# Kernel tuning notes

Measured on AMD Instinct MI355X. Metric: run time of the kernel, lower is better.

Reference implementation:

```python
import jax, jax.numpy as jnp
import numpy as np

NUM_HEADS = 16


def setup_inputs() -> dict:
    key = jax.random.key(0)
    k1, k2, k3 = jax.random.split(key, 3)
    B, L, H = 2, 2048, 1024
    return {
        "key": jax.random.normal(k1, (B, L, H), dtype=jnp.float32),
        "W_ctx": jax.random.normal(k2, (H, H), dtype=jnp.float32) * (1.0 / np.sqrt(H)),
        "b_ctx": jax.random.normal(k3, (H,), dtype=jnp.float32) * 0.01,
    }


def reference(key, W_ctx, b_ctx):
    # Note: the torch module defines q/k/v Linear layers but never calls them
    # in forward(); it reshapes the raw input into heads directly.
    B, L, H = key.shape
    dh = H // NUM_HEADS
    # [B, L, H] -> [B, nh, L, dh]
    x = key.reshape(B, L, NUM_HEADS, dh).transpose(0, 2, 1, 3)
    # QK^T then scale by sqrt(head_dim) (key.shape[-1] after head split)
    scores = jnp.einsum("bhqd,bhkd->bhqk", x, x) * (1.0 / np.float32(np.sqrt(dh)))
    attn = jax.nn.softmax(scores, axis=-1)  # dropout p treated as eval/identity
    ctx = jnp.einsum("bhqk,bhkd->bhqd", attn, x)
    # [B, nh, L, dh] -> [B, L, H]
    ctx = ctx.transpose(0, 2, 1, 3).reshape(B, L, H)
    # context_transform: nn.Linear(H, H, bias=True)
    return ctx @ W_ctx.T + b_ctx
```

## Files before the change

kernel.cpp:

```cpp
#include <hip/hip_runtime.h>
#include <stdint.h>

#define NH     16
#define LSEQ   2048
#define DH     64
#define HDIM   1024
#define BATCH  2

typedef __attribute__((ext_vector_type(8))) short bf16x8;
typedef __attribute__((ext_vector_type(4))) short bf16x4;
typedef __attribute__((ext_vector_type(8))) unsigned short u16x8;
typedef __attribute__((ext_vector_type(4))) float f32x4;

static __device__ inline unsigned short f2bs(float f) {
    union { float f; uint32_t u; } v; v.f = f;
    uint32_t u = v.u;
    return (unsigned short)((u + 0x7FFFu + ((u >> 16) & 1u)) >> 16);
}

#define GLOAD_LDS(gp, lp) \
    __builtin_amdgcn_global_load_lds((const __attribute__((address_space(1))) void*)(gp), \
                                     (__attribute__((address_space(3))) void*)(lp), 16, 0, 0)

#define QK_SCALE 0.42466083f

__global__ __launch_bounds__(256) void prep_kernel(const float* __restrict__ x,
                                                   const float* __restrict__ W,
                                                   unsigned short* __restrict__ xb,
                                                   unsigned short* __restrict__ xt,
                                                   unsigned short* __restrict__ wbt) {
    const int lt = blockIdx.x, bh = blockIdx.y;
    const int bid = bh * 32 + lt;
    const int t = threadIdx.x;

    if (t < 128) {
        const int gid = bid * 128 + t;
        const int n  = gid >> 7;
        const int kc = gid & 127;
        const float* src = W + (size_t)n * 1024 + kc * 8;
        float4 f0 = *(const float4*)(src);
        float4 f1 = *(const float4*)(src + 4);
        u16x8 v;
        v[0]=f2bs(f0.x); v[1]=f2bs(f0.y); v[2]=f2bs(f0.z); v[3]=f2bs(f0.w);
        v[4]=f2bs(f1.x); v[5]=f2bs(f1.y); v[6]=f2bs(f1.z); v[7]=f2bs(f1.w);
        const int nt = n >> 7, rn = n & 127;
        const int kt = kc >> 3, c = kc & 7;
        *(u16x8*)(wbt + (((size_t)nt * 16 + kt) * 128 + rn) * 64 + ((c ^ (rn & 7)) * 8)) = v;
    }

    const int b = bh >> 4, h = bh & 15;
    const int r = t >> 2, cp = t & 3;

    __shared__ __align__(16) unsigned short Sm[64][72];

    const float* src = x + ((size_t)(b * LSEQ + lt * 64 + r)) * HDIM + h * DH + cp * 16;
    float4 f0 = *(const float4*)(src);
    float4 f1 = *(const float4*)(src + 4);
    float4 f2 = *(const float4*)(src + 8);
    float4 f3 = *(const float4*)(src + 12);
    u16x8 lo, hi;
    lo[0]=f2bs(f0.x); lo[1]=f2bs(f0.y); lo[2]=f2bs(f0.z); lo[3]=f2bs(f0.w);
    lo[4]=f2bs(f1.x); lo[5]=f2bs(f1.y); lo[6]=f2bs(f1.z); lo[7]=f2bs(f1.w);
    hi[0]=f2bs(f2.x); hi[1]=f2bs(f2.y); hi[2]=f2bs(f2.z); hi[3]=f2bs(f2.w);
    hi[4]=f2bs(f3.x); hi[5]=f2bs(f3.y); hi[6]=f2bs(f3.z); hi[7]=f2bs(f3.w);
    u16x8 slo, shi;
    slo[0]=f2bs(f0.x*QK_SCALE); slo[1]=f2bs(f0.y*QK_SCALE); slo[2]=f2bs(f0.z*QK_SCALE); slo[3]=f2bs(f0.w*QK_SCALE);
    slo[4]=f2bs(f1.x*QK_SCALE); slo[5]=f2bs(f1.y*QK_SCALE); slo[6]=f2bs(f1.z*QK_SCALE); slo[7]=f2bs(f1.w*QK_SCALE);
    shi[0]=f2bs(f2.x*QK_SCALE); shi[1]=f2bs(f2.y*QK_SCALE); shi[2]=f2bs(f2.z*QK_SCALE); shi[3]=f2bs(f2.w*QK_SCALE);
    shi[4]=f2bs(f3.x*QK_SCALE); shi[5]=f2bs(f3.y*QK_SCALE); shi[6]=f2bs(f3.z*QK_SCALE); shi[7]=f2bs(f3.w*QK_SCALE);

    {
        unsigned short* kt = xb + ((size_t)bid) * 4096;
        const int s  = r >> 4, rla = r & 15;
        const int ks = cp >> 1, q0 = (cp & 1) * 2;
        *(u16x8*)(kt + ((s * 2 + ks) * 64 + q0 * 16 + rla) * 8)       = slo;
        *(u16x8*)(kt + ((s * 2 + ks) * 64 + (q0 + 1) * 16 + rla) * 8) = shi;
    }
    *(u16x8*)&Sm[r][cp * 16]     = lo;
    *(u16x8*)&Sm[r][cp * 16 + 8] = hi;
    __syncthreads();

    {
        const int dt = t >> 6, lane = t & 63;
        const int la = lane & 15, quad = lane >> 4;
        u16x8 g0, g1;
        #pragma unroll
        for (int kvt = 0; kvt < 2; ++kvt)
            #pragma unroll
            for (int j = 0; j < 4; ++j)
                g0[kvt * 4 + j] = Sm[kvt * 16 + quad * 4 + j][dt * 16 + la];
        #pragma unroll
        for (int kvt = 0; kvt < 2; ++kvt)
            #pragma unroll
            for (int j = 0; j < 4; ++j)
                g1[kvt * 4 + j] = Sm[(kvt + 2) * 16 + quad * 4 + j][dt * 16 + la];
        unsigned short* vt = xt + ((size_t)bid) * 4096;
        *(u16x8*)(vt + (dt * 64 + lane) * 16)     = g0;
        *(u16x8*)(vt + (dt * 64 + lane) * 16 + 8) = g1;
    }
}

__global__ __launch_bounds__(256) void attn_kernel(const unsigned short* __restrict__ xb,
                                                   const unsigned short* __restrict__ xt,
                                                   unsigned short* __restrict__ ctxt) {
    const int bh = blockIdx.x;
    const int qt = blockIdx.y;
    const int tid = threadIdx.x;
    const int w = tid >> 6, lane = tid & 63;
    const int la = lane & 15, quad = lane >> 4;

    __shared__ __align__(16) unsigned short KL[2][4096];
    __shared__ __align__(16) unsigned short VL[2][4096];

    const unsigned short* xbh = xb + (size_t)bh * 32 * 4096;
    const unsigned short* xth = xt + (size_t)bh * 32 * 4096;
    const int qbase = qt * 64 + w * 16;

    bf16x8 qf[2];
    {
        const unsigned short* qs = xbh + (qbase >> 6) * 4096 + (((qbase >> 4) & 3) * 2) * 512;
        qf[0] = *(const bf16x8*)(qs + lane * 8);
        qf[1] = *(const bf16x8*)(qs + 512 + lane * 8);
    }

    const f32x4 fzero = {0.f, 0.f, 0.f, 0.f};
    f32x4 acc[4];
    #pragma unroll
    for (int j = 0; j < 4; ++j) acc[j] = fzero;
    float lp = 0.f;

    const int soff = tid * 16;
    #pragma unroll
    for (int j = 0; j < 2; ++j) {
        const int off = j * 4096 + soff;
        GLOAD_LDS((const char*)xbh + off, (char*)KL[0] + off);
        GLOAD_LDS((const char*)xth + off, (char*)VL[0] + off);
    }
    __syncthreads();

    const char* kp = (const char*)xbh + 8192;
    const char* vp = (const char*)xth + 8192;

    for (int tt = 0; tt < 32; ++tt) {
        if (tt < 31) {
            char* kdst = (char*)KL[(tt + 1) & 1];
            GLOAD_LDS(kp + soff,        kdst + soff);
            GLOAD_LDS(kp + 4096 + soff, kdst + 4096 + soff);
        }

        const unsigned short* kb = KL[tt & 1];
        f32x4 st[4];
        #pragma unroll
        for (int kvt = 0; kvt < 4; ++kvt) {
            bf16x8 kf0 = *(const bf16x8*)(kb + (kvt * 2 + 0) * 512 + lane * 8);
            bf16x8 kf1 = *(const bf16x8*)(kb + (kvt * 2 + 1) * 512 + lane * 8);
            f32x4 s = fzero;
            s = __builtin_amdgcn_mfma_f32_16x16x32_bf16(kf0, qf[0], s, 0, 0, 0);
            s = __builtin_amdgcn_mfma_f32_16x16x32_bf16(kf1, qf[1], s, 0, 0, 0);
            st[kvt] = s;
        }

        bf16x4 pf[4];
        {
            float ls = 0.f;
            #pragma unroll
            for (int kvt = 0; kvt < 4; ++kvt) {
                float p0 = __builtin_amdgcn_exp2f(st[kvt][0]);
                float p1 = __builtin_amdgcn_exp2f(st[kvt][1]);
                float p2 = __builtin_amdgcn_exp2f(st[kvt][2]);
                float p3 = __builtin_amdgcn_exp2f(st[kvt][3]);
                ls += (p0 + p1) + (p2 + p3);
                union { uint2 u; bf16x4 v; } cv;
                cv.u = make_uint2(
                    __builtin_amdgcn_perm(__float_as_uint(p1), __float_as_uint(p0), 0x07060302),
                    __builtin_amdgcn_perm(__float_as_uint(p3), __float_as_uint(p2), 0x07060302));
                pf[kvt] = cv.v;
            }
            lp += ls;
        }

        __syncthreads();

        if (tt < 31) {
            char* vdst = (char*)VL[(tt + 1) & 1];
            GLOAD_LDS(vp + soff,        vdst + soff);
            GLOAD_LDS(vp + 4096 + soff, vdst + 4096 + soff);
            kp += 8192;
            vp += 8192;
        }

        const unsigned short* vb = VL[tt & 1];
        #pragma unroll
        for (int dt = 0; dt < 4; ++dt) {
            const unsigned short* vrow = vb + (dt * 64 + lane) * 16;
            bf16x4 vf0 = *(const bf16x4*)(vrow);
            bf16x4 vf1 = *(const bf16x4*)(vrow + 4);
            bf16x4 vf2 = *(const bf16x4*)(vrow + 8);
            bf16x4 vf3 = *(const bf16x4*)(vrow + 12);
            f32x4 a = acc[dt];
            a = __builtin_amdgcn_mfma_f32_16x16x16bf16_1k(vf0, pf[0], a, 0, 0, 0);
            a = __builtin_amdgcn_mfma_f32_16x16x16bf16_1k(vf1, pf[1], a, 0, 0, 0);
            a = __builtin_amdgcn_mfma_f32_16x16x16bf16_1k(vf2, pf[2], a, 0, 0, 0);
            a = __builtin_amdgcn_mfma_f32_16x16x16bf16_1k(vf3, pf[3], a, 0, 0, 0);
            acc[dt] = a;
        }
    }

    const int b = bh >> 4, h = bh & 15;
    const int mt = b * 16 + (qt >> 1);
    unsigned short* tbase = ctxt + ((size_t)mt * 16 + h) * 128 * 64;
    {
        float l = lp;
        l += __shfl_xor(l, 16);
        l += __shfl_xor(l, 32);
        const float inv = 1.0f / l;
        const int rr = (qt & 1) * 64 + w * 16 + la;
        unsigned short* rowp = tbase + rr * 64 + (quad & 1) * 4;
        #pragma unroll
        for (int dt = 0; dt < 4; ++dt) {
            f32x4 a = acc[dt];
            const int c = dt * 2 + (quad >> 1);
            *(ushort4*)(rowp + ((c ^ (rr & 7)) * 8)) =
                make_ushort4(f2bs(a[0] * inv), f2bs(a[1] * inv),
                             f2bs(a[2] * inv), f2bs(a[3] * inv));
        }
    }
}

__global__ __launch_bounds__(256) void proj_kernel(const unsigned short* __restrict__ ctxt,
                                                   const unsigned short* __restrict__ wbt,
                                                   const float* __restrict__ bias,
                                                   float* __restrict__ out) {
    const int ntb = blockIdx.x;
    const int mtb = blockIdx.y;
    const int tid = threadIdx.x;
    const int w = tid >> 6, lane = tid & 63;
    const int la = lane & 15, quad = lane >> 4;
    const int wm = (w >> 1) * 64, wn = (w & 1) * 64;

    __shared__ __align__(16) unsigned short As[2][8192];
    __shared__ __align__(16) unsigned short Bs[2][8192];

    const unsigned short* abase = ctxt + (size_t)mtb * 16 * 8192;
    const unsigned short* bbase = wbt  + (size_t)ntb * 16 * 8192;

    const int sw0 = ((quad)     ^ (la & 7)) * 8;
    const int sw1 = ((quad + 4) ^ (la & 7)) * 8;

    const f32x4 fzero = {0.f, 0.f, 0.f, 0.f};
    f32x4 acc[4][4];
    #pragma unroll
    for (int i = 0; i < 4; ++i)
        #pragma unroll
        for (int j = 0; j < 4; ++j) acc[i][j] = fzero;

    #pragma unroll
    for (int j = 0; j < 4; ++j) {
        const int fc = j * 256 + tid;
        GLOAD_LDS((const char*)abase + fc * 16, (char*)As[0] + fc * 16);
        GLOAD_LDS((const char*)bbase + fc * 16, (char*)Bs[0] + fc * 16);
    }
    __syncthreads();

    for (int kt = 0; kt < 16; ++kt) {
        if (kt < 15) {
            const char* asrc = (const char*)(abase + (kt + 1) * 8192);
            const char* bsrc = (const char*)(bbase + (kt + 1) * 8192);
            char* adst = (char*)As[(kt + 1) & 1];
            char* bdst = (char*)Bs[(kt + 1) & 1];
            #pragma unroll
            for (int j = 0; j < 4; ++j) {
                const int fc = j * 256 + tid;
                GLOAD_LDS(asrc + fc * 16, adst + fc * 16);
                GLOAD_LDS(bsrc + fc * 16, bdst + fc * 16);
            }
        }

        const unsigned short* Ab = As[kt & 1];
        const unsigned short* Bb = Bs[kt & 1];
        #pragma unroll
        for (int ks2 = 0; ks2 < 2; ++ks2) {
            const int sw = ks2 ? sw1 : sw0;
            bf16x8 af[4], bfr[4];
            #pragma unroll
            for (int mt = 0; mt < 4; ++mt) af[mt]  = *(const bf16x8*)&Ab[(wm + mt * 16 + la) * 64 + sw];
            #pragma unroll
            for (int nt = 0; nt < 4; ++nt) bfr[nt] = *(const bf16x8*)&Bb[(wn + nt * 16 + la) * 64 + sw];
            #pragma unroll
            for (int mt = 0; mt < 4; ++mt)
                #pragma unroll
                for (int nt = 0; nt < 4; ++nt)
                    acc[mt][nt] = __builtin_amdgcn_mfma_f32_16x16x32_bf16(af[mt], bfr[nt], acc[mt][nt], 0, 0, 0);
        }
        __syncthreads();
    }

    const int m0 = mtb * 128, n0 = ntb * 128;
    #pragma unroll
    for (int nt = 0; nt < 4; ++nt) {
        const int n = n0 + wn + nt * 16 + la;
        const float bv = bias[n];
        #pragma unroll
        for (int mt = 0; mt < 4; ++mt)
            #pragma unroll
            for (int r = 0; r < 4; ++r) {
                const int m = m0 + wm + mt * 16 + quad * 4 + r;
                out[(size_t)m * HDIM + n] = acc[mt][nt][r] + bv;
            }
    }
}

extern "C" void kernel_launch(void* const* d_in, const int* in_sizes, int n_in,
                              void* d_out, int out_size, void* d_ws, size_t ws_size,
                              hipStream_t stream) {
    const float* x    = (const float*)d_in[0];
    const float* W    = (const float*)d_in[1];
    const float* bias = (const float*)d_in[2];
    float* out = (float*)d_out;

    unsigned short* ctxt = (unsigned short*)d_ws;
    unsigned short* xbp  = (unsigned short*)((char*)d_ws + ( 8u << 20));
    unsigned short* xtp  = (unsigned short*)((char*)d_ws + (16u << 20));
    unsigned short* wbt  = (unsigned short*)((char*)d_ws + (24u << 20));

    prep_kernel<<<dim3(32, 32), 256, 0, stream>>>(x, W, xbp, xtp, wbt);
    attn_kernel<<<dim3(32, 32), 256, 0, stream>>>(xbp, xtp, ctxt);
    proj_kernel<<<dim3(8, 32), 256, 0, stream>>>(ctxt, wbt, bias, out);
}
```

Baseline: 148.2 us.

## Process two query tiles per wave in attention and swizzle V layout

Each wave now handles 32 query rows (two 16-row MFMA tiles) instead of 16, so each K and V fragment loaded from LDS is reused for two tiles. The attention grid is halved to 16 query blocks of 128 rows. The transposed V layout written by prep gets an XOR swizzle on its 4-element groups, and attn reads it with the matching swizzle, to cut LDS bank conflicts. In exchange the kernel uses more registers for accumulators and launches fewer workgroups, which may lower occupancy.

```diff
diff --git a/kernel.cpp b/kernel.cpp
--- a/kernel.cpp
+++ b/kernel.cpp
@@ -83,20 +83,18 @@
     {
         const int dt = t >> 6, lane = t & 63;
         const int la = lane & 15, quad = lane >> 4;
-        u16x8 g0, g1;
-        #pragma unroll
-        for (int kvt = 0; kvt < 2; ++kvt)
-            #pragma unroll
-            for (int j = 0; j < 4; ++j)
-                g0[kvt * 4 + j] = Sm[kvt * 16 + quad * 4 + j][dt * 16 + la];
-        #pragma unroll
-        for (int kvt = 0; kvt < 2; ++kvt)
-            #pragma unroll
-            for (int j = 0; j < 4; ++j)
-                g1[kvt * 4 + j] = Sm[(kvt + 2) * 16 + quad * 4 + j][dt * 16 + la];
+        const int sw = (lane >> 2) & 3;
         unsigned short* vt = xt + ((size_t)bid) * 4096;
-        *(u16x8*)(vt + (dt * 64 + lane) * 16)     = g0;
-        *(u16x8*)(vt + (dt * 64 + lane) * 16 + 8) = g1;
+        unsigned short* row = vt + (dt * 64 + lane) * 16;
+        #pragma unroll
+        for (int g = 0; g < 4; ++g) {
+            ushort4 fr;
+            fr.x = Sm[g * 16 + quad * 4 + 0][dt * 16 + la];
+            fr.y = Sm[g * 16 + quad * 4 + 1][dt * 16 + la];
+            fr.z = Sm[g * 16 + quad * 4 + 2][dt * 16 + la];
+            fr.w = Sm[g * 16 + quad * 4 + 3][dt * 16 + la];
+            *(ushort4*)(row + ((g ^ sw) * 4)) = fr;
+        }
     }
 }
 
@@ -108,26 +106,29 @@
     const int tid = threadIdx.x;
     const int w = tid >> 6, lane = tid & 63;
     const int la = lane & 15, quad = lane >> 4;
+    const int vsw = (lane >> 2) & 3;
 
     __shared__ __align__(16) unsigned short KL[2][4096];
     __shared__ __align__(16) unsigned short VL[2][4096];
 
     const unsigned short* xbh = xb + (size_t)bh * 32 * 4096;
     const unsigned short* xth = xt + (size_t)bh * 32 * 4096;
-    const int qbase = qt * 64 + w * 16;
-
-    bf16x8 qf[2];
+    const int qbase = qt * 128 + w * 32;
+
+    bf16x8 qf[2][2];
     {
-        const unsigned short* qs = xbh + (qbase >> 6) * 4096 + (((qbase >> 4) & 3) * 2) * 512;
-        qf[0] = *(const bf16x8*)(qs + lane * 8);
-        qf[1] = *(const bf16x8*)(qs + 512 + lane * 8);
+        const unsigned short* qs = xbh + (qbase >> 6) * 4096 + ((qbase >> 4) & 3) * 1024;
+        qf[0][0] = *(const bf16x8*)(qs + lane * 8);
+        qf[0][1] = *(const bf16x8*)(qs + 512 + lane * 8);
+        qf[1][0] = *(const bf16x8*)(qs + 1024 + lane * 8);
+        qf[1][1] = *(const bf16x8*)(qs + 1536 + lane * 8);
     }
 
     const f32x4 fzero = {0.f, 0.f, 0.f, 0.f};
-    f32x4 acc[4];
-    #pragma unroll
-    for (int j = 0; j < 4; ++j) acc[j] = fzero;
-    float lp = 0.f;
+    f32x4 acc0[4], acc1[4];
+    #pragma unroll
+    for (int j = 0; j < 4; ++j) { acc0[j] = fzero; acc1[j] = fzero; }
+    float lp0 = 0.f, lp1 = 0.f;
 
     const int soff = tid * 16;
     #pragma unroll
@@ -149,34 +150,46 @@
         }
 
         const unsigned short* kb = KL[tt & 1];
-        f32x4 st[4];
-        #pragma unroll
-        for (int kvt = 0; kvt < 4; ++kvt) {
-            bf16x8 kf0 = *(const bf16x8*)(kb + (kvt * 2 + 0) * 512 + lane * 8);
-            bf16x8 kf1 = *(const bf16x8*)(kb + (kvt * 2 + 1) * 512 + lane * 8);
-            f32x4 s = fzero;
-            s = __builtin_amdgcn_mfma_f32_16x16x32_bf16(kf0, qf[0], s, 0, 0, 0);
-            s = __builtin_amdgcn_mfma_f32_16x16x32_bf16(kf1, qf[1], s, 0, 0, 0);
-            st[kvt] = s;
-        }
-
-        bf16x4 pf[4];
+        bf16x4 pf0[4], pf1[4];
         {
-            float ls = 0.f;
+            float ls0 = 0.f, ls1 = 0.f;
             #pragma unroll
             for (int kvt = 0; kvt < 4; ++kvt) {
-                float p0 = __builtin_amdgcn_exp2f(st[kvt][0]);
-                float p1 = __builtin_amdgcn_exp2f(st[kvt][1]);
-                float p2 = __builtin_amdgcn_exp2f(st[kvt][2]);
-                float p3 = __builtin_amdgcn_exp2f(st[kvt][3]);
-                ls += (p0 + p1) + (p2 + p3);
-                union { uint2 u; bf16x4 v; } cv;
-                cv.u = make_uint2(
-                    __builtin_amdgcn_perm(__float_as_uint(p1), __float_as_uint(p0), 0x07060302),
-                    __builtin_amdgcn_perm(__float_as_uint(p3), __float_as_uint(p2), 0x07060302));
-                pf[kvt] = cv.v;
+                bf16x8 kf0 = *(const bf16x8*)(kb + (kvt * 2 + 0) * 512 + lane * 8);
+                bf16x8 kf1 = *(const bf16x8*)(kb + (kvt * 2 + 1) * 512 + lane * 8);
+                f32x4 s0 = fzero, s1 = fzero;
+                s0 = __builtin_amdgcn_mfma_f32_16x16x32_bf16(kf0, qf[0][0], s0, 0, 0, 0);
+                s0 = __builtin_amdgcn_mfma_f32_16x16x32_bf16(kf1, qf[0][1], s0, 0, 0, 0);
+                s1 = __builtin_amdgcn_mfma_f32_16x16x32_bf16(kf0, qf[1][0], s1, 0, 0, 0);
+                s1 = __builtin_amdgcn_mfma_f32_16x16x32_bf16(kf1, qf[1][1], s1, 0, 0, 0);
+
+                {
+                    float p0 = __builtin_amdgcn_exp2f(s0[0]);
+                    float p1 = __builtin_amdgcn_exp2f(s0[1]);
+                    float p2 = __builtin_amdgcn_exp2f(s0[2]);
+                    float p3 = __builtin_amdgcn_exp2f(s0[3]);
+                    ls0 += (p0 + p1) + (p2 + p3);
+                    union { uint2 u; bf16x4 v; } cv;
+                    cv.u = make_uint2(
+                        __builtin_amdgcn_perm(__float_as_uint(p1), __float_as_uint(p0), 0x07060302),
+                        __builtin_amdgcn_perm(__float_as_uint(p3), __float_as_uint(p2), 0x07060302));
+                    pf0[kvt] = cv.v;
+                }
+                {
+                    float p0 = __builtin_amdgcn_exp2f(s1[0]);
+                    float p1 = __builtin_amdgcn_exp2f(s1[1]);
+                    float p2 = __builtin_amdgcn_exp2f(s1[2]);
+                    float p3 = __builtin_amdgcn_exp2f(s1[3]);
+                    ls1 += (p0 + p1) + (p2 + p3);
+                    union { uint2 u; bf16x4 v; } cv;
+                    cv.u = make_uint2(
+                        __builtin_amdgcn_perm(__float_as_uint(p1), __float_as_uint(p0), 0x07060302),
+                        __builtin_amdgcn_perm(__float_as_uint(p3), __float_as_uint(p2), 0x07060302));
+                    pf1[kvt] = cv.v;
+                }
             }
-            lp += ls;
+            lp0 += ls0;
+            lp1 += ls1;
         }
 
         __syncthreads();
@@ -193,36 +206,56 @@
         #pragma unroll
         for (int dt = 0; dt < 4; ++dt) {
             const unsigned short* vrow = vb + (dt * 64 + lane) * 16;
-            bf16x4 vf0 = *(const bf16x4*)(vrow);
-            bf16x4 vf1 = *(const bf16x4*)(vrow + 4);
-            bf16x4 vf2 = *(const bf16x4*)(vrow + 8);
-            bf16x4 vf3 = *(const bf16x4*)(vrow + 12);
-            f32x4 a = acc[dt];
-            a = __builtin_amdgcn_mfma_f32_16x16x16bf16_1k(vf0, pf[0], a, 0, 0, 0);
-            a = __builtin_amdgcn_mfma_f32_16x16x16bf16_1k(vf1, pf[1], a, 0, 0, 0);
-            a = __builtin_amdgcn_mfma_f32_16x16x16bf16_1k(vf2, pf[2], a, 0, 0, 0);
-            a = __builtin_amdgcn_mfma_f32_16x16x16bf16_1k(vf3, pf[3], a, 0, 0, 0);
-            acc[dt] = a;
+            bf16x4 vf0 = *(const bf16x4*)(vrow + ((0 ^ vsw) * 4));
+            bf16x4 vf1 = *(const bf16x4*)(vrow + ((1 ^ vsw) * 4));
+            bf16x4 vf2 = *(const bf16x4*)(vrow + ((2 ^ vsw) * 4));
+            bf16x4 vf3 = *(const bf16x4*)(vrow + ((3 ^ vsw) * 4));
+            f32x4 a0 = acc0[dt], a1 = acc1[dt];
+            a0 = __builtin_amdgcn_mfma_f32_16x16x16bf16_1k(vf0, pf0[0], a0, 0, 0, 0);
+            a0 = __builtin_amdgcn_mfma_f32_16x16x16bf16_1k(vf1, pf0[1], a0, 0, 0, 0);
+            a0 = __builtin_amdgcn_mfma_f32_16x16x16bf16_1k(vf2, pf0[2], a0, 0, 0, 0);
+            a0 = __builtin_amdgcn_mfma_f32_16x16x16bf16_1k(vf3, pf0[3], a0, 0, 0, 0);
+            a1 = __builtin_amdgcn_mfma_f32_16x16x16bf16_1k(vf0, pf1[0], a1, 0, 0, 0);
+            a1 = __builtin_amdgcn_mfma_f32_16x16x16bf16_1k(vf1, pf1[1], a1, 0, 0, 0);
+            a1 = __builtin_amdgcn_mfma_f32_16x16x16bf16_1k(vf2, pf1[2], a1, 0, 0, 0);
+            a1 = __builtin_amdgcn_mfma_f32_16x16x16bf16_1k(vf3, pf1[3], a1, 0, 0, 0);
+            acc0[dt] = a0;
+            acc1[dt] = a1;
         }
     }
 
     const int b = bh >> 4, h = bh & 15;
-    const int mt = b * 16 + (qt >> 1);
+    const int mt = b * 16 + qt;
     unsigned short* tbase = ctxt + ((size_t)mt * 16 + h) * 128 * 64;
     {
-        float l = lp;
-        l += __shfl_xor(l, 16);
-        l += __shfl_xor(l, 32);
-        const float inv = 1.0f / l;
-        const int rr = (qt & 1) * 64 + w * 16 + la;
-        unsigned short* rowp = tbase + rr * 64 + (quad & 1) * 4;
+        float l0 = lp0;
+        l0 += __shfl_xor(l0, 16);
+        l0 += __shfl_xor(l0, 32);
+        float l1 = lp1;
+        l1 += __shfl_xor(l1, 16);
+        l1 += __shfl_xor(l1, 32);
+        const float inv0 = 1.0f / l0;
+        const float inv1 = 1.0f / l1;
+
+        const int rr0 = w * 32 + la;
+        unsigned short* rowp0 = tbase + rr0 * 64 + (quad & 1) * 4;
         #pragma unroll
         for (int dt = 0; dt < 4; ++dt) {
-            f32x4 a = acc[dt];
+            f32x4 a = acc0[dt];
             const int c = dt * 2 + (quad >> 1);
-            *(ushort4*)(rowp + ((c ^ (rr & 7)) * 8)) =
-                make_ushort4(f2bs(a[0] * inv), f2bs(a[1] * inv),
-                             f2bs(a[2] * inv), f2bs(a[3] * inv));
+            *(ushort4*)(rowp0 + ((c ^ (rr0 & 7)) * 8)) =
+                make_ushort4(f2bs(a[0] * inv0), f2bs(a[1] * inv0),
+                             f2bs(a[2] * inv0), f2bs(a[3] * inv0));
+        }
+        const int rr1 = w * 32 + 16 + la;
+        unsigned short* rowp1 = tbase + rr1 * 64 + (quad & 1) * 4;
+        #pragma unroll
+        for (int dt = 0; dt < 4; ++dt) {
+            f32x4 a = acc1[dt];
+            const int c = dt * 2 + (quad >> 1);
+            *(ushort4*)(rowp1 + ((c ^ (rr1 & 7)) * 8)) =
+                make_ushort4(f2bs(a[0] * inv1), f2bs(a[1] * inv1),
+                             f2bs(a[2] * inv1), f2bs(a[3] * inv1));
         }
     }
 }
@@ -324,6 +357,6 @@
     unsigned short* wbt  = (unsigned short*)((char*)d_ws + (24u << 20));
 
     prep_kernel<<<dim3(32, 32), 256, 0, stream>>>(x, W, xbp, xtp, wbt);
-    attn_kernel<<<dim3(32, 32), 256, 0, stream>>>(xbp, xtp, ctxt);
+    attn_kernel<<<dim3(32, 16), 256, 0, stream>>>(xbp, xtp, ctxt);
     proj_kernel<<<dim3(8, 32), 256, 0, stream>>>(ctxt, wbt, bias, out);
 }
```

After: 154.2 us. 1.04x slower.

## Rewrite attention with 32x32x16 MFMA, 128-row query tiles and 4-deep LDS pipeline

Applied to the files above, without the earlier changes.

Switches the attention inner loop from 16x16 MFMA tiles to 32x32x16 bf16 MFMA, with each block now covering 128 query rows, so the grid is halved. K and V are stored in a row-major, XOR-swizzled layout, and P fragments are built with cvt_pk_bf16 plus permlane32_swap. K/V tiles are prefetched two steps ahead into a 4-buffer LDS ring using explicit vmcnt waits, and MFMA sections run at raised priority. The aim is to cut LDS traffic per FLOP, reduce barriers and hide load latency. The cost is more registers (two f32x16 accumulators plus score tiles), more LDS, and fewer blocks.

```diff
diff --git a/kernel.cpp b/kernel.cpp
--- a/kernel.cpp
+++ b/kernel.cpp
@@ -11,6 +11,7 @@
 typedef __attribute__((ext_vector_type(4))) short bf16x4;
 typedef __attribute__((ext_vector_type(8))) unsigned short u16x8;
 typedef __attribute__((ext_vector_type(4))) float f32x4;
+typedef __attribute__((ext_vector_type(16))) float f32x16;
 
 static __device__ inline unsigned short f2bs(float f) {
     union { float f; uint32_t u; } v; v.f = f;
@@ -18,9 +19,20 @@
     return (unsigned short)((u + 0x7FFFu + ((u >> 16) & 1u)) >> 16);
 }
 
+static __device__ inline unsigned int cvtpk(float lo, float hi) {
+    unsigned int r;
+    asm("v_cvt_pk_bf16_f32 %0, %1, %2" : "=v"(r) : "v"(lo), "v"(hi));
+    return r;
+}
+static __device__ inline void pl32swap(unsigned int &a, unsigned int &b) {
+    asm volatile("v_permlane32_swap_b32 %0, %1" : "+v"(a), "+v"(b));
+}
+
 #define GLOAD_LDS(gp, lp) \
     __builtin_amdgcn_global_load_lds((const __attribute__((address_space(1))) void*)(gp), \
                                      (__attribute__((address_space(3))) void*)(lp), 16, 0, 0)
+
+#define MFMA32(A, B, C) __builtin_amdgcn_mfma_f32_32x32x16_bf16((A), (B), (C), 0, 0, 0)
 
 #define QK_SCALE 0.42466083f
 
@@ -70,33 +82,26 @@
     shi[4]=f2bs(f3.x*QK_SCALE); shi[5]=f2bs(f3.y*QK_SCALE); shi[6]=f2bs(f3.z*QK_SCALE); shi[7]=f2bs(f3.w*QK_SCALE);
 
     {
-        unsigned short* kt = xb + ((size_t)bid) * 4096;
-        const int s  = r >> 4, rla = r & 15;
-        const int ks = cp >> 1, q0 = (cp & 1) * 2;
-        *(u16x8*)(kt + ((s * 2 + ks) * 64 + q0 * 16 + rla) * 8)       = slo;
-        *(u16x8*)(kt + ((s * 2 + ks) * 64 + (q0 + 1) * 16 + rla) * 8) = shi;
+        unsigned short* xrow = xb + (size_t)bid * 4096 + r * 64;
+        const int xrs = (r & 7) * 8;
+        *(u16x8*)(xrow + ((cp * 16 + 0) ^ xrs)) = slo;
+        *(u16x8*)(xrow + ((cp * 16 + 8) ^ xrs)) = shi;
     }
     *(u16x8*)&Sm[r][cp * 16]     = lo;
     *(u16x8*)&Sm[r][cp * 16 + 8] = hi;
     __syncthreads();
 
     {
-        const int dt = t >> 6, lane = t & 63;
-        const int la = lane & 15, quad = lane >> 4;
+        const int d = t >> 2, part = (t & 3) * 16;
+        unsigned short* vrow = xt + (size_t)bid * 4096 + d * 64;
+        const int xrs = (d & 7) * 8;
         u16x8 g0, g1;
         #pragma unroll
-        for (int kvt = 0; kvt < 2; ++kvt)
-            #pragma unroll
-            for (int j = 0; j < 4; ++j)
-                g0[kvt * 4 + j] = Sm[kvt * 16 + quad * 4 + j][dt * 16 + la];
-        #pragma unroll
-        for (int kvt = 0; kvt < 2; ++kvt)
-            #pragma unroll
-            for (int j = 0; j < 4; ++j)
-                g1[kvt * 4 + j] = Sm[(kvt + 2) * 16 + quad * 4 + j][dt * 16 + la];
-        unsigned short* vt = xt + ((size_t)bid) * 4096;
-        *(u16x8*)(vt + (dt * 64 + lane) * 16)     = g0;
-        *(u16x8*)(vt + (dt * 64 + lane) * 16 + 8) = g1;
+        for (int i = 0; i < 8; ++i) g0[i] = Sm[part + i][d];
+        #pragma unroll
+        for (int i = 0; i < 8; ++i) g1[i] = Sm[part + 8 + i][d];
+        *(u16x8*)(vrow + ((part + 0) ^ xrs)) = g0;
+        *(u16x8*)(vrow + ((part + 8) ^ xrs)) = g1;
     }
 }
 
@@ -107,123 +112,149 @@
     const int qt = blockIdx.y;
     const int tid = threadIdx.x;
     const int w = tid >> 6, lane = tid & 63;
-    const int la = lane & 15, quad = lane >> 4;
-
-    __shared__ __align__(16) unsigned short KL[2][4096];
-    __shared__ __align__(16) unsigned short VL[2][4096];
-
-    const unsigned short* xbh = xb + (size_t)bh * 32 * 4096;
-    const unsigned short* xth = xt + (size_t)bh * 32 * 4096;
-    const int qbase = qt * 64 + w * 16;
-
-    bf16x8 qf[2];
+    const int l31 = lane & 31, hh = lane >> 5;
+
+    __shared__ __align__(16) unsigned short KL[4][4096];
+    __shared__ __align__(16) unsigned short VL[4][4096];
+
+    const char* xbB = (const char*)(xb + (size_t)bh * 32 * 4096);
+    const char* xtB = (const char*)(xt + (size_t)bh * 32 * 4096);
+
+    bf16x8 qf[4];
     {
-        const unsigned short* qs = xbh + (qbase >> 6) * 4096 + (((qbase >> 4) & 3) * 2) * 512;
-        qf[0] = *(const bf16x8*)(qs + lane * 8);
-        qf[1] = *(const bf16x8*)(qs + 512 + lane * 8);
-    }
-
-    const f32x4 fzero = {0.f, 0.f, 0.f, 0.f};
-    f32x4 acc[4];
-    #pragma unroll
-    for (int j = 0; j < 4; ++j) acc[j] = fzero;
+        const int qtile = qt * 2 + (w >> 1);
+        const int rq = (w & 1) * 32 + l31;
+        const char* qbase = xbB + (size_t)qtile * 8192 + rq * 128;
+        const int qxr = (rq & 7) << 4;
+        #pragma unroll
+        for (int ds = 0; ds < 4; ++ds)
+            qf[ds] = *(const bf16x8*)(qbase + ((ds * 32 + hh * 16) ^ qxr));
+    }
+
+    f32x16 accA, accB;
+    #pragma unroll
+    for (int r = 0; r < 16; ++r) { accA[r] = 0.f; accB[r] = 0.f; }
     float lp = 0.f;
 
     const int soff = tid * 16;
     #pragma unroll
     for (int j = 0; j < 2; ++j) {
-        const int off = j * 4096 + soff;
-        GLOAD_LDS((const char*)xbh + off, (char*)KL[0] + off);
-        GLOAD_LDS((const char*)xth + off, (char*)VL[0] + off);
-    }
-    __syncthreads();
-
-    const char* kp = (const char*)xbh + 8192;
-    const char* vp = (const char*)xth + 8192;
+        const char* kps = xbB + j * 8192;
+        const char* vps = xtB + j * 8192;
+        GLOAD_LDS(kps + soff,        (char*)KL[j] + soff);
+        GLOAD_LDS(kps + 4096 + soff, (char*)KL[j] + 4096 + soff);
+        GLOAD_LDS(vps + soff,        (char*)VL[j] + soff);
+        GLOAD_LDS(vps + 4096 + soff, (char*)VL[j] + 4096 + soff);
+    }
+    asm volatile("s_waitcnt vmcnt(4)" ::: "memory");
+    __builtin_amdgcn_s_barrier();
+
+    const int kxr = (l31 & 7) << 4;
 
     for (int tt = 0; tt < 32; ++tt) {
-        if (tt < 31) {
-            char* kdst = (char*)KL[(tt + 1) & 1];
-            GLOAD_LDS(kp + soff,        kdst + soff);
-            GLOAD_LDS(kp + 4096 + soff, kdst + 4096 + soff);
-        }
-
-        const unsigned short* kb = KL[tt & 1];
-        f32x4 st[4];
-        #pragma unroll
-        for (int kvt = 0; kvt < 4; ++kvt) {
-            bf16x8 kf0 = *(const bf16x8*)(kb + (kvt * 2 + 0) * 512 + lane * 8);
-            bf16x8 kf1 = *(const bf16x8*)(kb + (kvt * 2 + 1) * 512 + lane * 8);
-            f32x4 s = fzero;
-            s = __builtin_amdgcn_mfma_f32_16x16x32_bf16(kf0, qf[0], s, 0, 0, 0);
-            s = __builtin_amdgcn_mfma_f32_16x16x32_bf16(kf1, qf[1], s, 0, 0, 0);
-            st[kvt] = s;
-        }
-
-        bf16x4 pf[4];
+        if (tt < 30) {
+            const char* kps = xbB + (tt + 2) * 8192;
+            const char* vps = xtB + (tt + 2) * 8192;
+            char* kdst = (char*)KL[(tt + 2) & 3];
+            char* vdst = (char*)VL[(tt + 2) & 3];
+            GLOAD_LDS(kps + soff,        kdst + soff);
+            GLOAD_LDS(kps + 4096 + soff, kdst + 4096 + soff);
+            GLOAD_LDS(vps + soff,        vdst + soff);
+            GLOAD_LDS(vps + 4096 + soff, vdst + 4096 + soff);
+        }
+
+        const char* kb0 = (const char*)KL[tt & 3] + l31 * 128;
+        const char* kb1 = kb0 + 4096;
+        f32x16 s0, s1;
+        #pragma unroll
+        for (int r = 0; r < 16; ++r) { s0[r] = 0.f; s1[r] = 0.f; }
+        __builtin_amdgcn_s_setprio(1);
+        #pragma unroll
+        for (int ds = 0; ds < 4; ++ds) {
+            const int off = (ds * 32 + hh * 16) ^ kxr;
+            bf16x8 kfa = *(const bf16x8*)(kb0 + off);
+            bf16x8 kfb = *(const bf16x8*)(kb1 + off);
+            s0 = MFMA32(kfa, qf[ds], s0);
+            s1 = MFMA32(kfb, qf[ds], s1);
+        }
+        __builtin_amdgcn_s_setprio(0);
+
+        f32x16 e0, e1;
         {
             float ls = 0.f;
             #pragma unroll
-            for (int kvt = 0; kvt < 4; ++kvt) {
-                float p0 = __builtin_amdgcn_exp2f(st[kvt][0]);
-                float p1 = __builtin_amdgcn_exp2f(st[kvt][1]);
-                float p2 = __builtin_amdgcn_exp2f(st[kvt][2]);
-                float p3 = __builtin_amdgcn_exp2f(st[kvt][3]);
-                ls += (p0 + p1) + (p2 + p3);
-                union { uint2 u; bf16x4 v; } cv;
-                cv.u = make_uint2(
-                    __builtin_amdgcn_perm(__float_as_uint(p1), __float_as_uint(p0), 0x07060302),
-                    __builtin_amdgcn_perm(__float_as_uint(p3), __float_as_uint(p2), 0x07060302));
-                pf[kvt] = cv.v;
+            for (int r = 0; r < 16; ++r) {
+                e0[r] = __builtin_amdgcn_exp2f(s0[r]);
+                e1[r] = __builtin_amdgcn_exp2f(s1[r]);
+                ls += e0[r] + e1[r];
             }
             lp += ls;
         }
-
-        __syncthreads();
-
-        if (tt < 31) {
-            char* vdst = (char*)VL[(tt + 1) & 1];
-            GLOAD_LDS(vp + soff,        vdst + soff);
-            GLOAD_LDS(vp + 4096 + soff, vdst + 4096 + soff);
-            kp += 8192;
-            vp += 8192;
-        }
-
-        const unsigned short* vb = VL[tt & 1];
-        #pragma unroll
-        for (int dt = 0; dt < 4; ++dt) {
-            const unsigned short* vrow = vb + (dt * 64 + lane) * 16;
-            bf16x4 vf0 = *(const bf16x4*)(vrow);
-            bf16x4 vf1 = *(const bf16x4*)(vrow + 4);
-            bf16x4 vf2 = *(const bf16x4*)(vrow + 8);
-            bf16x4 vf3 = *(const bf16x4*)(vrow + 12);
-            f32x4 a = acc[dt];
-            a = __builtin_amdgcn_mfma_f32_16x16x16bf16_1k(vf0, pf[0], a, 0, 0, 0);
-            a = __builtin_amdgcn_mfma_f32_16x16x16bf16_1k(vf1, pf[1], a, 0, 0, 0);
-            a = __builtin_amdgcn_mfma_f32_16x16x16bf16_1k(vf2, pf[2], a, 0, 0, 0);
-            a = __builtin_amdgcn_mfma_f32_16x16x16bf16_1k(vf3, pf[3], a, 0, 0, 0);
-            acc[dt] = a;
-        }
-    }
-
-    const int b = bh >> 4, h = bh & 15;
-    const int mt = b * 16 + (qt >> 1);
-    unsigned short* tbase = ctxt + ((size_t)mt * 16 + h) * 128 * 64;
-    {
-        float l = lp;
-        l += __shfl_xor(l, 16);
-        l += __shfl_xor(l, 32);
-        const float inv = 1.0f / l;
-        const int rr = (qt & 1) * 64 + w * 16 + la;
-        unsigned short* rowp = tbase + rr * 64 + (quad & 1) * 4;
-        #pragma unroll
-        for (int dt = 0; dt < 4; ++dt) {
-            f32x4 a = acc[dt];
-            const int c = dt * 2 + (quad >> 1);
-            *(ushort4*)(rowp + ((c ^ (rr & 7)) * 8)) =
-                make_ushort4(f2bs(a[0] * inv), f2bs(a[1] * inv),
-                             f2bs(a[2] * inv), f2bs(a[3] * inv));
-        }
+        bf16x8 pa[4];
+        #pragma unroll
+        for (int ks = 0; ks < 4; ++ks) {
+            const int r0 = (ks & 1) * 8;
+            unsigned int x0, y0, x1, y1;
+            if (ks < 2) {
+                x0 = cvtpk(e0[r0 + 0], e0[r0 + 1]);
+                y0 = cvtpk(e0[r0 + 4], e0[r0 + 5]);
+                x1 = cvtpk(e0[r0 + 2], e0[r0 + 3]);
+                y1 = cvtpk(e0[r0 + 6], e0[r0 + 7]);
+            } else {
+                x0 = cvtpk(e1[r0 + 0], e1[r0 + 1]);
+                y0 = cvtpk(e1[r0 + 4], e1[r0 + 5]);
+                x1 = cvtpk(e1[r0 + 2], e1[r0 + 3]);
+                y1 = cvtpk(e1[r0 + 6], e1[r0 + 7]);
+            }
+            pl32swap(x0, y0);
+            pl32swap(x1, y1);
+            union { unsigned int u[4]; bf16x8 v; } pu;
+            pu.u[0] = x0; pu.u[1] = x1; pu.u[2] = y0; pu.u[3] = y1;
+            pa[ks] = pu.v;
+        }
+
+        if (tt < 30) {
+            asm volatile("s_waitcnt vmcnt(4)" ::: "memory");
+        } else {
+            asm volatile("s_waitcnt vmcnt(0)" ::: "memory");
+        }
+        __builtin_amdgcn_s_barrier();
+
+        const char* vb0 = (const char*)VL[tt & 3] + l31 * 128;
+        const char* vb1 = vb0 + 4096;
+        __builtin_amdgcn_s_setprio(1);
+        #pragma unroll
+        for (int ks = 0; ks < 4; ++ks) {
+            const int off = (ks * 32 + hh * 16) ^ kxr;
+            bf16x8 vfa = *(const bf16x8*)(vb0 + off);
+            bf16x8 vfb = *(const bf16x8*)(vb1 + off);
+            accA = MFMA32(pa[ks], vfa, accA);
+            accB = MFMA32(pa[ks], vfb, accB);
+        }
+        __builtin_amdgcn_s_setprio(0);
+    }
+
+    lp += __shfl_xor(lp, 32);
+    const float inv = 1.0f / lp;
+    __syncthreads();
+    float* invL = (float*)KL;
+    invL[w * 32 + l31] = inv;
+    __syncthreads();
+
+    const int b = bh >> 4, hd = bh & 15;
+    const int mt = b * 16 + qt;
+    unsigned short* tbase = ctxt + ((size_t)mt * 16 + hd) * 128 * 64;
+    const int col0 = l31, col1 = 32 + l31;
+    const int c80 = col0 >> 3, c81 = col1 >> 3, ce = col0 & 7;
+    #pragma unroll
+    for (int r = 0; r < 16; ++r) {
+        const int crow = (r & 3) + 8 * (r >> 2) + 4 * hh;
+        const float iv = invL[w * 32 + crow];
+        const int rr = w * 32 + crow;
+        unsigned short* rowp = tbase + rr * 64;
+        const int sw = rr & 7;
+        rowp[((c80 ^ sw) * 8) + ce] = f2bs(accA[r] * iv);
+        rowp[((c81 ^ sw) * 8) + ce] = f2bs(accB[r] * iv);
     }
 }
 
@@ -324,6 +355,6 @@
     unsigned short* wbt  = (unsigned short*)((char*)d_ws + (24u << 20));
 
     prep_kernel<<<dim3(32, 32), 256, 0, stream>>>(x, W, xbp, xtp, wbt);
-    attn_kernel<<<dim3(32, 32), 256, 0, stream>>>(xbp, xtp, ctxt);
+    attn_kernel<<<dim3(32, 16), 256, 0, stream>>>(xbp, xtp, ctxt);
     proj_kernel<<<dim3(8, 32), 256, 0, stream>>>(ctxt, wbt, bias, out);
 }
```

After: 144.3 us. -2.6%, faster.
